# Performance work log

Measured on AMD Instinct MI355X. Metric: run time of the kernel, lower is better.

Reference implementation:

```python
import jax, jax.numpy as jnp
import numpy as np
from jax import lax

K = 2000      # node_num of GraphConvolution
H, W = 75, 100  # edge_region_feature spatial grid (from per-pixel concat loops)


def setup_inputs() -> dict:
    key = jax.random.key(0)
    k1, k2, k3, k4 = jax.random.split(key, 4)
    b, c = 8, 512
    edge_region_feature = jax.random.normal(k1, (b, c, H, W), dtype=jnp.float32)
    edge_region_predict = jax.random.normal(k2, (b, 3, H, W), dtype=jnp.float32)
    # GraphConvolution params: kaiming_normal_(fan_out) weights, zero bias
    w1 = jax.random.normal(k3, (512, 128), dtype=jnp.float32) * np.sqrt(2.0 / 128)
    b1 = jnp.zeros((K, 128), dtype=jnp.float32)
    w2 = jax.random.normal(k4, (128, 128), dtype=jnp.float32) * np.sqrt(2.0 / 128)
    b2 = jnp.zeros((K, 128), dtype=jnp.float32)
    return {"edge_region_feature": edge_region_feature,
            "edge_region_predict": edge_region_predict,
            "w1": w1, "b1": b1, "w2": w2, "b2": b2}


def reference(edge_region_feature, edge_region_predict, w1, b1, w2, b2):
    b, c = edge_region_feature.shape[0], edge_region_feature.shape[1]
    # block_feature built as: for x in range(W) for y in range(H) -> node n at (y=n%H, x=n//H)
    block = jnp.transpose(edge_region_feature, (0, 3, 2, 1)).reshape(b, W * H, c)  # (b, 7500, 512)

    # topk over channel-0 prediction, flattened row-major (idx = y*W + x)
    scores = edge_region_predict[:, 0, :, :].reshape(b, -1)            # (b, 7500)
    _vals, topk_idx = lax.top_k(scores, K)
    sorted_idx = jnp.sort(topk_idx, axis=1)                            # (b, 2000) int32

    # gather node features (replicates original's indexing of block_feature)
    node_map = jnp.take_along_axis(block, sorted_idx[:, :, None], axis=1)  # (b, 2000, 512)

    # generate_adjacent_map: decode positions with width=W, connect 8-neighborhood (+self)
    py = sorted_idx // W
    px = sorted_idx % W
    near_y = jnp.abs(py[:, :, None] - py[:, None, :]) <= 1
    near_x = jnp.abs(px[:, :, None] - px[:, None, :]) <= 1
    adj = (near_y & near_x).astype(jnp.float32)                        # (b, 2000, 2000)

    # node_feature_grouping = ReLU6 -> GCN(512->128) -> GCN(128->128)
    inp = jnp.clip(jnp.concatenate([adj, node_map], axis=2), 0.0, 6.0)  # ReLU6 on cat(adj, nodes)
    a = inp[:, :, :K]
    nf = inp[:, :, K:]
    # GCN1: A @ X @ W1 + b1  (in!=out -> no residual)
    x1 = jnp.einsum('bij,bjf->bif', a, nf) @ w1 + b1                   # (b, 2000, 128)
    # GCN2: A @ X1 @ W2 + b2 + X1 (in==out -> residual)
    x2 = jnp.einsum('bij,bjf->bif', a, x1) @ w2 + b2 + x1              # (b, 2000, 128)

    node_output_feature = jnp.tanh(x2)
    return node_output_feature, sorted_idx
```

## Files before the change

kernel.cpp:

```cpp
#include <hip/hip_runtime.h>
#include <cmath>

#define H_DIM 75
#define W_DIM 100
#define HW 7500
#define KSEL 2000
#define BATCH 8
#define CIN 512
#define FDIM 128

typedef short v4s __attribute__((ext_vector_type(4)));
typedef short v8s __attribute__((ext_vector_type(8)));
typedef float v16f __attribute__((ext_vector_type(16)));

__device__ __forceinline__ unsigned int map_key(float f) {
  unsigned int u = __float_as_uint(f);
  return (u & 0x80000000u) ? ~u : (u | 0x80000000u);
}

__device__ __forceinline__ float fast_tanh(float x) {
  float e = __expf(2.0f * x);
  return 1.0f - 2.0f * __builtin_amdgcn_rcpf(e + 1.0f);
}

__device__ __forceinline__ unsigned short bf16_rne(float v) {
  unsigned int u = __float_as_uint(v);
  unsigned int r = u + 0x7FFFu + ((u >> 16) & 1u);
  return (unsigned short)(r >> 16);
}
__device__ __forceinline__ float bf16_to_f(unsigned short h) {
  return __uint_as_float(((unsigned int)h) << 16);
}

__global__ __launch_bounds__(1024) void topk_nbr_kernel(
    const float* __restrict__ pred, const float* __restrict__ w1,
    const float* __restrict__ w2,
    int* __restrict__ off_ws, float* __restrict__ out_idx,
    unsigned short* __restrict__ nbr, unsigned char* __restrict__ cnt,
    unsigned short* __restrict__ w1t_hi, unsigned short* __restrict__ w1t_lo,
    unsigned short* __restrict__ w2t_hi, unsigned short* __restrict__ w2t_lo)
{
  __shared__ unsigned int keys[HW];
  __shared__ unsigned int whist[16 * 256];
  __shared__ unsigned int hist[256];
  __shared__ unsigned int partials[16];
  __shared__ unsigned int s_prefix, s_kth;
  const int tid = threadIdx.x;

  if (blockIdx.x >= BATCH) {
    int base = (blockIdx.x - BATCH) * 1024 + tid;
    for (int e = base; e < CIN * FDIM + FDIM * FDIM; e += 8 * 1024) {
      if (e < CIN * FDIM) {
        int k = e & (CIN - 1), f = e >> 9;
        float v = w1[k * FDIM + f];
        unsigned short hi = bf16_rne(v);
        unsigned short lo = bf16_rne(v - bf16_to_f(hi));
        w1t_hi[(size_t)f * CIN + k] = hi;
        w1t_lo[(size_t)f * CIN + k] = lo;
      } else {
        int e2 = e - CIN * FDIM;
        int k = e2 & (FDIM - 1), f = e2 >> 7;
        float v = w2[k * FDIM + f];
        unsigned short hi = bf16_rne(v);
        unsigned short lo = bf16_rne(v - bf16_to_f(hi));
        w2t_hi[(size_t)f * FDIM + k] = hi;
        w2t_lo[(size_t)f * FDIM + k] = lo;
      }
    }
    return;
  }

  const int b = blockIdx.x;
  const int lane = tid & 63, w = tid >> 6;
  const float* scores = pred + (size_t)b * 3 * HW;
  for (int i = tid; i < HW; i += 1024) keys[i] = map_key(scores[i]);
  if (tid == 0) { s_prefix = 0u; s_kth = KSEL; }
  __syncthreads();

  for (int shift = 24; shift >= 0; shift -= 8) {
    for (int i = tid; i < 16 * 256; i += 1024) whist[i] = 0u;
    __syncthreads();
    unsigned int pref = s_prefix;
    unsigned int maskhi = (shift == 24) ? 0u : (0xFFFFFFFFu << (shift + 8));
    for (int i = tid; i < HW; i += 1024) {
      unsigned int k = keys[i];
      if ((k & maskhi) == pref)
        atomicAdd(&whist[w * 256 + ((k >> shift) & 0xFFu)], 1u);
    }
    __syncthreads();
    if (tid < 256) {
      unsigned int s = 0;
      #pragma unroll
      for (int ww = 0; ww < 16; ++ww) s += whist[ww * 256 + tid];
      hist[tid] = s;
    }
    __syncthreads();
    if (tid < 64) {
      unsigned int b0 = hist[tid * 4], b1 = hist[tid * 4 + 1];
      unsigned int b2 = hist[tid * 4 + 2], b3 = hist[tid * 4 + 3];
      unsigned int kth = s_kth;
      unsigned int T = b0 + b1 + b2 + b3;
      #pragma unroll
      for (int off = 1; off < 64; off <<= 1) {
        unsigned int t = __shfl_down(T, off, 64);
        if (tid + off < 64) T += t;
      }
      unsigned int U = __shfl_down(T, 1, 64);
      if (tid == 63) U = 0u;
      unsigned int s3 = b3 + U, s2 = b2 + s3, s1 = b1 + s2, s0 = b0 + s1;
      if (s0 >= kth && s1 < kth) { s_prefix = pref | ((unsigned)(4 * tid + 0) << shift); s_kth = kth - s1; }
      if (s1 >= kth && s2 < kth) { s_prefix = pref | ((unsigned)(4 * tid + 1) << shift); s_kth = kth - s2; }
      if (s2 >= kth && s3 < kth) { s_prefix = pref | ((unsigned)(4 * tid + 2) << shift); s_kth = kth - s3; }
      if (s3 >= kth && U  < kth) { s_prefix = pref | ((unsigned)(4 * tid + 3) << shift); s_kth = kth - U; }
    }
    __syncthreads();
  }
  const unsigned int thresh = s_prefix;

  unsigned int local[8];
  unsigned int sum = 0;
  #pragma unroll
  for (int e = 0; e < 8; ++e) {
    int i = tid * 8 + e;
    unsigned int p = 0;
    if (i < HW) {
      unsigned int ky = keys[i];
      if (ky > thresh) p = 1u;
      else if (ky == thresh) p = (1u << 16);
    }
    local[e] = p; sum += p;
  }
  __syncthreads();
  short* pos_of  = (short*)keys;
  int*   s_idx_sh = (int*)((char*)keys + 15000);
  for (int i = tid; i < HW; i += 1024) pos_of[i] = -1;

  unsigned int inc = sum;
  #pragma unroll
  for (int off = 1; off < 64; off <<= 1) {
    unsigned int t = __shfl_up(inc, off, 64);
    if (lane >= off) inc += t;
  }
  if (lane == 63) partials[w] = inc;
  __syncthreads();
  if (tid < 16) {
    unsigned int v = partials[tid];
    #pragma unroll
    for (int off = 1; off < 16; off <<= 1) {
      unsigned int t = __shfl_up(v, off, 64);
      if (tid >= off) v += t;
    }
    partials[tid] = v;
  }
  __syncthreads();
  unsigned int total = partials[15];
  unsigned int run = (w ? partials[w - 1] : 0u) + inc - sum;
  unsigned int ties = (unsigned int)KSEL - (total & 0xFFFFu);
  #pragma unroll
  for (int e = 0; e < 8; ++e) {
    int i = tid * 8 + e;
    unsigned int p = local[e];
    unsigned int gt_pref = run & 0xFFFFu;
    unsigned int eq_pref = run >> 16;
    bool sel = (p & 1u) || (((p >> 16) != 0u) && eq_pref < ties);
    if (sel) {
      unsigned int pos = gt_pref + (eq_pref < ties ? eq_pref : ties);
      off_ws[b * KSEL + pos] = (i % H_DIM) * W_DIM + i / H_DIM;
      out_idx[b * KSEL + pos] = (float)i;
      s_idx_sh[pos] = i;
      pos_of[i] = (short)pos;
    }
    run += p;
  }
  __syncthreads();

  for (int i = tid; i < KSEL; i += 1024) {
    int q = s_idx_sh[i];
    int py = q / W_DIM, px = q % W_DIM;
    unsigned short tmp[9];
    int c = 0;
    #pragma unroll
    for (int dy = -1; dy <= 1; ++dy) {
      int y = py + dy;
      if ((unsigned)y >= (unsigned)H_DIM) continue;
      #pragma unroll
      for (int dx = -1; dx <= 1; ++dx) {
        int x = px + dx;
        if ((unsigned)x >= (unsigned)W_DIM) continue;
        short p = pos_of[y * W_DIM + x];
        if (p >= 0) tmp[c++] = (unsigned short)p;
      }
    }
    #pragma unroll
    for (int t = 0; t < 9; ++t)
      nbr[(size_t)(b * KSEL + i) * 9 + t] = (t < c) ? tmp[t] : (unsigned short)0;
    cnt[b * KSEL + i] = (unsigned char)c;
  }
}

__global__ __launch_bounds__(512) void gather_kernel(
    const float* __restrict__ feat, const int* __restrict__ off_ws,
    unsigned short* __restrict__ nft_hi, unsigned short* __restrict__ nft_lo)
{
  __shared__ __align__(16) float s_plane[HW];
  const int b = blockIdx.y;
  const int c = blockIdx.x;
  const int tid = threadIdx.x;
  const float4* p4 = (const float4*)(feat + ((size_t)b * CIN + c) * HW);
  float4* sp4 = (float4*)s_plane;
  #pragma unroll
  for (int i = tid; i < HW / 4; i += 512)
    sp4[i] = p4[i];
  __syncthreads();
  if (tid < KSEL / 4) {
    const uint4* o4 = (const uint4*)off_ws + (size_t)b * (KSEL / 4);
    uint4 o = o4[tid];
    float v0 = fminf(fmaxf(s_plane[o.x], 0.f), 6.f);
    float v1 = fminf(fmaxf(s_plane[o.y], 0.f), 6.f);
    float v2 = fminf(fmaxf(s_plane[o.z], 0.f), 6.f);
    float v3 = fminf(fmaxf(s_plane[o.w], 0.f), 6.f);
    ushort4 h, l;
    h.x = bf16_rne(v0); l.x = bf16_rne(v0 - bf16_to_f(h.x));
    h.y = bf16_rne(v1); l.y = bf16_rne(v1 - bf16_to_f(h.y));
    h.z = bf16_rne(v2); l.z = bf16_rne(v2 - bf16_to_f(h.z));
    h.w = bf16_rne(v3); l.w = bf16_rne(v3 - bf16_to_f(h.w));
    size_t row = ((size_t)b * CIN + c) * KSEL;
    ((ushort4*)&nft_hi[row])[tid] = h;
    ((ushort4*)&nft_lo[row])[tid] = l;
  }
}

__global__ __launch_bounds__(256) void gemm1_mfma(
    const unsigned short* __restrict__ nft_hi,
    const unsigned short* __restrict__ nft_lo,
    const unsigned short* __restrict__ w1t_hi,
    const unsigned short* __restrict__ w1t_lo,
    float* __restrict__ G)
{
  __shared__ unsigned short a_hi[2][64][20], a_lo[2][64][20];
  const int b = blockIdx.y;
  const int n0 = blockIdx.x * 64;
  const int tid = threadIdx.x;
  const int lane = tid & 63, w = tid >> 6;
  const int wr = w & 1, wc = w >> 1;
  const int q = lane >> 5, m = lane & 31;
  v16f acc0, acc1;
  #pragma unroll
  for (int i = 0; i < 16; ++i) { acc0[i] = 0.f; acc1[i] = 0.f; }
  const unsigned short* nh = nft_hi + (size_t)b * CIN * KSEL;
  const unsigned short* nl = nft_lo + (size_t)b * CIN * KSEL;
  const int an = wr * 32 + m;
  const int f0 = wc * 64 + m;
  const int n_st = tid & 63, ks = (tid >> 6) * 4;

  #pragma unroll
  for (int j = 0; j < 4; ++j) {
    size_t gi = (size_t)(ks + j) * KSEL + n0 + n_st;
    a_hi[0][n_st][ks + j] = nh[gi];
    a_lo[0][n_st][ks + j] = nl[gi];
  }
  __syncthreads();

  for (int k0 = 0; k0 < CIN; k0 += 16) {
    const int p = (k0 >> 4) & 1;
    if (k0 + 16 < CIN) {
      #pragma unroll
      for (int j = 0; j < 4; ++j) {
        size_t gi = (size_t)(k0 + 16 + ks + j) * KSEL + n0 + n_st;
        a_hi[p ^ 1][n_st][ks + j] = nh[gi];
        a_lo[p ^ 1][n_st][ks + j] = nl[gi];
      }
    }
    v4s ah0 = *(const v4s*)&a_hi[p][an][q * 8];
    v4s ah1 = *(const v4s*)&a_hi[p][an][q * 8 + 4];
    v4s al0 = *(const v4s*)&a_lo[p][an][q * 8];
    v4s al1 = *(const v4s*)&a_lo[p][an][q * 8 + 4];
    v8s avh = __builtin_shufflevector(ah0, ah1, 0, 1, 2, 3, 4, 5, 6, 7);
    v8s avl = __builtin_shufflevector(al0, al1, 0, 1, 2, 3, 4, 5, 6, 7);
    v8s b0h = *(const v8s*)&w1t_hi[(size_t)f0 * CIN + k0 + q * 8];
    v8s b0l = *(const v8s*)&w1t_lo[(size_t)f0 * CIN + k0 + q * 8];
    v8s b1h = *(const v8s*)&w1t_hi[(size_t)(f0 + 32) * CIN + k0 + q * 8];
    v8s b1l = *(const v8s*)&w1t_lo[(size_t)(f0 + 32) * CIN + k0 + q * 8];
    acc0 = __builtin_amdgcn_mfma_f32_32x32x16_bf16(avh, b0h, acc0, 0, 0, 0);
    acc0 = __builtin_amdgcn_mfma_f32_32x32x16_bf16(avh, b0l, acc0, 0, 0, 0);
    acc0 = __builtin_amdgcn_mfma_f32_32x32x16_bf16(avl, b0h, acc0, 0, 0, 0);
    acc1 = __builtin_amdgcn_mfma_f32_32x32x16_bf16(avh, b1h, acc1, 0, 0, 0);
    acc1 = __builtin_amdgcn_mfma_f32_32x32x16_bf16(avh, b1l, acc1, 0, 0, 0);
    acc1 = __builtin_amdgcn_mfma_f32_32x32x16_bf16(avl, b1h, acc1, 0, 0, 0);
    __syncthreads();
  }
  float* ob = G + (size_t)b * KSEL * FDIM;
  #pragma unroll
  for (int reg = 0; reg < 16; ++reg) {
    int row = n0 + wr * 32 + (reg & 3) + 8 * (reg >> 2) + 4 * q;
    if (row < KSEL) {
      ob[(size_t)row * FDIM + f0]      = acc0[reg];
      ob[(size_t)row * FDIM + f0 + 32] = acc1[reg];
    }
  }
}

__global__ __launch_bounds__(256) void x1_kernel(
    const float* __restrict__ G, const float* __restrict__ b1,
    const unsigned short* __restrict__ nbr, const unsigned char* __restrict__ cnt,
    float* __restrict__ x1, unsigned short* __restrict__ x1h,
    unsigned short* __restrict__ x1l)
{
  const int g = threadIdx.x >> 5, lane = threadIdx.x & 31;
  const int node = blockIdx.x * 8 + g;
  const int bb = blockIdx.y;
  const size_t bi = (size_t)bb * KSEL + node;
  const unsigned short* nb = nbr + bi * 9;
  unsigned short idx[9];
  #pragma unroll
  for (int t = 0; t < 9; ++t) idx[t] = nb[t];
  const int c = cnt[bi];
  const float4* G4 = (const float4*)G + (size_t)bb * KSEL * 32;
  float4 v[9];
  #pragma unroll
  for (int t = 0; t < 9; ++t) v[t] = G4[(size_t)idx[t] * 32 + lane];
  float4 acc = ((const float4*)b1)[node * 32 + lane];
  #pragma unroll
  for (int t = 0; t < 9; ++t) {
    float mk = (t < c) ? 1.f : 0.f;
    acc.x = fmaf(v[t].x, mk, acc.x);
    acc.y = fmaf(v[t].y, mk, acc.y);
    acc.z = fmaf(v[t].z, mk, acc.z);
    acc.w = fmaf(v[t].w, mk, acc.w);
  }
  ((float4*)x1)[bi * 32 + lane] = acc;
  ushort4 h, l;
  h.x = bf16_rne(acc.x); l.x = bf16_rne(acc.x - bf16_to_f(h.x));
  h.y = bf16_rne(acc.y); l.y = bf16_rne(acc.y - bf16_to_f(h.y));
  h.z = bf16_rne(acc.z); l.z = bf16_rne(acc.z - bf16_to_f(h.z));
  h.w = bf16_rne(acc.w); l.w = bf16_rne(acc.w - bf16_to_f(h.w));
  ((ushort4*)x1h)[bi * 32 + lane] = h;
  ((ushort4*)x1l)[bi * 32 + lane] = l;
}

__global__ __launch_bounds__(256) void gemm2_mfma(
    const unsigned short* __restrict__ x1h,
    const unsigned short* __restrict__ x1l,
    const unsigned short* __restrict__ w2t_hi,
    const unsigned short* __restrict__ w2t_lo,
    float* __restrict__ Hm)
{
  const int b = blockIdx.y;
  const int n0 = blockIdx.x * 64;
  const int tid = threadIdx.x;
  const int lane = tid & 63, w = tid >> 6;
  const int wr = w & 1, wc = w >> 1;
  const int q = lane >> 5, m = lane & 31;
  int arow = n0 + wr * 32 + m;
  if (arow > KSEL - 1) arow = KSEL - 1;
  const unsigned short* xh = x1h + ((size_t)b * KSEL + arow) * FDIM;
  const unsigned short* xl = x1l + ((size_t)b * KSEL + arow) * FDIM;
  const int f0 = wc * 64 + m;
  v16f acc0, acc1;
  #pragma unroll
  for (int i = 0; i < 16; ++i) { acc0[i] = 0.f; acc1[i] = 0.f; }
  #pragma unroll
  for (int k0 = 0; k0 < FDIM; k0 += 16) {
    v8s avh = *(const v8s*)&xh[k0 + q * 8];
    v8s avl = *(const v8s*)&xl[k0 + q * 8];
    v8s b0h = *(const v8s*)&w2t_hi[(size_t)f0 * FDIM + k0 + q * 8];
    v8s b0l = *(const v8s*)&w2t_lo[(size_t)f0 * FDIM + k0 + q * 8];
    v8s b1h = *(const v8s*)&w2t_hi[(size_t)(f0 + 32) * FDIM + k0 + q * 8];
    v8s b1l = *(const v8s*)&w2t_lo[(size_t)(f0 + 32) * FDIM + k0 + q * 8];
    acc0 = __builtin_amdgcn_mfma_f32_32x32x16_bf16(avh, b0h, acc0, 0, 0, 0);
    acc0 = __builtin_amdgcn_mfma_f32_32x32x16_bf16(avh, b0l, acc0, 0, 0, 0);
    acc0 = __builtin_amdgcn_mfma_f32_32x32x16_bf16(avl, b0h, acc0, 0, 0, 0);
    acc1 = __builtin_amdgcn_mfma_f32_32x32x16_bf16(avh, b1h, acc1, 0, 0, 0);
    acc1 = __builtin_amdgcn_mfma_f32_32x32x16_bf16(avh, b1l, acc1, 0, 0, 0);
    acc1 = __builtin_amdgcn_mfma_f32_32x32x16_bf16(avl, b1h, acc1, 0, 0, 0);
  }
  float* ob = Hm + (size_t)b * KSEL * FDIM;
  #pragma unroll
  for (int reg = 0; reg < 16; ++reg) {
    int row = n0 + wr * 32 + (reg & 3) + 8 * (reg >> 2) + 4 * q;
    if (row < KSEL) {
      ob[(size_t)row * FDIM + f0]      = acc0[reg];
      ob[(size_t)row * FDIM + f0 + 32] = acc1[reg];
    }
  }
}

__global__ __launch_bounds__(256) void out_kernel(
    const float* __restrict__ Hm, const float* __restrict__ x1,
    const float* __restrict__ b2,
    const unsigned short* __restrict__ nbr, const unsigned char* __restrict__ cnt,
    float* __restrict__ out)
{
  const int g = threadIdx.x >> 5, lane = threadIdx.x & 31;
  const int node = blockIdx.x * 8 + g;
  const int bb = blockIdx.y;
  const size_t bi = (size_t)bb * KSEL + node;
  const unsigned short* nb = nbr + bi * 9;
  unsigned short idx[9];
  #pragma unroll
  for (int t = 0; t < 9; ++t) idx[t] = nb[t];
  const int c = cnt[bi];
  const float4* H4 = (const float4*)Hm + (size_t)bb * KSEL * 32;
  float4 v[9];
  #pragma unroll
  for (int t = 0; t < 9; ++t) v[t] = H4[(size_t)idx[t] * 32 + lane];
  float4 acc = ((const float4*)b2)[node * 32 + lane];
  float4 xv = ((const float4*)x1)[bi * 32 + lane];
  acc.x += xv.x; acc.y += xv.y; acc.z += xv.z; acc.w += xv.w;
  #pragma unroll
  for (int t = 0; t < 9; ++t) {
    float mk = (t < c) ? 1.f : 0.f;
    acc.x = fmaf(v[t].x, mk, acc.x);
    acc.y = fmaf(v[t].y, mk, acc.y);
    acc.z = fmaf(v[t].z, mk, acc.z);
    acc.w = fmaf(v[t].w, mk, acc.w);
  }
  float4 r;
  r.x = fast_tanh(acc.x); r.y = fast_tanh(acc.y);
  r.z = fast_tanh(acc.z); r.w = fast_tanh(acc.w);
  ((float4*)out)[bi * 32 + lane] = r;
}

extern "C" void kernel_launch(void* const* d_in, const int* in_sizes, int n_in,
                              void* d_out, int out_size, void* d_ws, size_t ws_size,
                              hipStream_t stream) {
  const float* feat = (const float*)d_in[0];
  const float* pred = (const float*)d_in[1];
  const float* w1   = (const float*)d_in[2];
  const float* b1   = (const float*)d_in[3];
  const float* w2   = (const float*)d_in[4];
  const float* b2   = (const float*)d_in[5];
  float* out0 = (float*)d_out;
  float* out_idx = out0 + (size_t)BATCH * KSEL * FDIM;

  char* ws = (char*)d_ws;
  int*            off_ws = (int*)(ws + 0);
  unsigned short* nbr    = (unsigned short*)(ws + 64256);
  unsigned char*  cnt    = (unsigned char*)(ws + 352512);
  float*          G      = (float*)(ws + 368640);
  char*           R      = ws + 8560640;
  unsigned short* nft_hi = (unsigned short*)R;
  unsigned short* nft_lo = (unsigned short*)(R + 16384000);
  unsigned short* w1t_hi = (unsigned short*)(R + 32768256);
  unsigned short* w1t_lo = (unsigned short*)(R + 32899328);
  unsigned short* w2t_hi = (unsigned short*)(R + 33030656);
  unsigned short* w2t_lo = (unsigned short*)(R + 33063424);
  float*          x1     = (float*)R;
  float*          Hm     = (float*)(R + 8388608);
  unsigned short* x1h    = (unsigned short*)(R + 16777216);
  unsigned short* x1l    = (unsigned short*)(R + 20873472);

  topk_nbr_kernel<<<BATCH + 8, 1024, 0, stream>>>(
      pred, w1, w2, off_ws, out_idx, nbr, cnt, w1t_hi, w1t_lo, w2t_hi, w2t_lo);
  gather_kernel<<<dim3(CIN, BATCH), 512, 0, stream>>>(feat, off_ws, nft_hi, nft_lo);
  gemm1_mfma<<<dim3(32, BATCH), 256, 0, stream>>>(nft_hi, nft_lo, w1t_hi, w1t_lo, G);
  x1_kernel<<<dim3(KSEL / 8, BATCH), 256, 0, stream>>>(G, b1, nbr, cnt, x1, x1h, x1l);
  gemm2_mfma<<<dim3(32, BATCH), 256, 0, stream>>>(x1h, x1l, w2t_hi, w2t_lo, Hm);
  out_kernel<<<dim3(KSEL / 8, BATCH), 256, 0, stream>>>(Hm, x1, b2, nbr, cnt, out0);
}
```

Measured before the change: 263.7 us.

## Fuse feature gather into GEMM1 and sparse aggregation into GEMM2

Removes the separate gather kernel: GEMM1 now reads the selected node features directly from the input tensor via the offset table, applies ReLU6 and splits them into bf16 hi/lo in-register before staging to shared memory. It also folds the x1 neighbor-aggregation kernel into GEMM2, which builds the bf16 x1 tile in XOR-swizzled shared memory instead of round-tripping through global buffers. This cuts two launches and the large nft_hi/nft_lo intermediate writes and reads. The cost is that GEMM1's A loads become strided scalar reads (stride HW floats per channel) from the original feature layout, with only 256 blocks doing that gathering work.

```diff
diff --git a/kernel.cpp b/kernel.cpp
--- a/kernel.cpp
+++ b/kernel.cpp
@@ -198,41 +198,8 @@
   }
 }
 
-__global__ __launch_bounds__(512) void gather_kernel(
+__global__ __launch_bounds__(256) void gemm1_fused(
     const float* __restrict__ feat, const int* __restrict__ off_ws,
-    unsigned short* __restrict__ nft_hi, unsigned short* __restrict__ nft_lo)
-{
-  __shared__ __align__(16) float s_plane[HW];
-  const int b = blockIdx.y;
-  const int c = blockIdx.x;
-  const int tid = threadIdx.x;
-  const float4* p4 = (const float4*)(feat + ((size_t)b * CIN + c) * HW);
-  float4* sp4 = (float4*)s_plane;
-  #pragma unroll
-  for (int i = tid; i < HW / 4; i += 512)
-    sp4[i] = p4[i];
-  __syncthreads();
-  if (tid < KSEL / 4) {
-    const uint4* o4 = (const uint4*)off_ws + (size_t)b * (KSEL / 4);
-    uint4 o = o4[tid];
-    float v0 = fminf(fmaxf(s_plane[o.x], 0.f), 6.f);
-    float v1 = fminf(fmaxf(s_plane[o.y], 0.f), 6.f);
-    float v2 = fminf(fmaxf(s_plane[o.z], 0.f), 6.f);
-    float v3 = fminf(fmaxf(s_plane[o.w], 0.f), 6.f);
-    ushort4 h, l;
-    h.x = bf16_rne(v0); l.x = bf16_rne(v0 - bf16_to_f(h.x));
-    h.y = bf16_rne(v1); l.y = bf16_rne(v1 - bf16_to_f(h.y));
-    h.z = bf16_rne(v2); l.z = bf16_rne(v2 - bf16_to_f(h.z));
-    h.w = bf16_rne(v3); l.w = bf16_rne(v3 - bf16_to_f(h.w));
-    size_t row = ((size_t)b * CIN + c) * KSEL;
-    ((ushort4*)&nft_hi[row])[tid] = h;
-    ((ushort4*)&nft_lo[row])[tid] = l;
-  }
-}
-
-__global__ __launch_bounds__(256) void gemm1_mfma(
-    const unsigned short* __restrict__ nft_hi,
-    const unsigned short* __restrict__ nft_lo,
     const unsigned short* __restrict__ w1t_hi,
     const unsigned short* __restrict__ w1t_lo,
     float* __restrict__ G)
@@ -247,17 +214,20 @@
   v16f acc0, acc1;
   #pragma unroll
   for (int i = 0; i < 16; ++i) { acc0[i] = 0.f; acc1[i] = 0.f; }
-  const unsigned short* nh = nft_hi + (size_t)b * CIN * KSEL;
-  const unsigned short* nl = nft_lo + (size_t)b * CIN * KSEL;
   const int an = wr * 32 + m;
   const int f0 = wc * 64 + m;
   const int n_st = tid & 63, ks = (tid >> 6) * 4;
+  int nidx = n0 + n_st;
+  if (nidx > KSEL - 1) nidx = KSEL - 1;
+  const float* fb = feat + (size_t)b * CIN * HW + off_ws[b * KSEL + nidx];
 
   #pragma unroll
   for (int j = 0; j < 4; ++j) {
-    size_t gi = (size_t)(ks + j) * KSEL + n0 + n_st;
-    a_hi[0][n_st][ks + j] = nh[gi];
-    a_lo[0][n_st][ks + j] = nl[gi];
+    float v = fb[(size_t)(ks + j) * HW];
+    v = fminf(fmaxf(v, 0.f), 6.f);
+    unsigned short hi = bf16_rne(v);
+    a_hi[0][n_st][ks + j] = hi;
+    a_lo[0][n_st][ks + j] = bf16_rne(v - bf16_to_f(hi));
   }
   __syncthreads();
 
@@ -266,9 +236,11 @@
     if (k0 + 16 < CIN) {
       #pragma unroll
       for (int j = 0; j < 4; ++j) {
-        size_t gi = (size_t)(k0 + 16 + ks + j) * KSEL + n0 + n_st;
-        a_hi[p ^ 1][n_st][ks + j] = nh[gi];
-        a_lo[p ^ 1][n_st][ks + j] = nl[gi];
+        float v = fb[(size_t)(k0 + 16 + ks + j) * HW];
+        v = fminf(fmaxf(v, 0.f), 6.f);
+        unsigned short hi = bf16_rne(v);
+        a_hi[p ^ 1][n_st][ks + j] = hi;
+        a_lo[p ^ 1][n_st][ks + j] = bf16_rne(v - bf16_to_f(hi));
       }
     }
     v4s ah0 = *(const v4s*)&a_hi[p][an][q * 8];
@@ -300,69 +272,69 @@
   }
 }
 
-__global__ __launch_bounds__(256) void x1_kernel(
+__global__ __launch_bounds__(256) void gemm2_fused(
     const float* __restrict__ G, const float* __restrict__ b1,
     const unsigned short* __restrict__ nbr, const unsigned char* __restrict__ cnt,
-    float* __restrict__ x1, unsigned short* __restrict__ x1h,
-    unsigned short* __restrict__ x1l)
-{
-  const int g = threadIdx.x >> 5, lane = threadIdx.x & 31;
-  const int node = blockIdx.x * 8 + g;
-  const int bb = blockIdx.y;
-  const size_t bi = (size_t)bb * KSEL + node;
-  const unsigned short* nb = nbr + bi * 9;
-  unsigned short idx[9];
-  #pragma unroll
-  for (int t = 0; t < 9; ++t) idx[t] = nb[t];
-  const int c = cnt[bi];
-  const float4* G4 = (const float4*)G + (size_t)bb * KSEL * 32;
-  float4 v[9];
-  #pragma unroll
-  for (int t = 0; t < 9; ++t) v[t] = G4[(size_t)idx[t] * 32 + lane];
-  float4 acc = ((const float4*)b1)[node * 32 + lane];
-  #pragma unroll
-  for (int t = 0; t < 9; ++t) {
-    float mk = (t < c) ? 1.f : 0.f;
-    acc.x = fmaf(v[t].x, mk, acc.x);
-    acc.y = fmaf(v[t].y, mk, acc.y);
-    acc.z = fmaf(v[t].z, mk, acc.z);
-    acc.w = fmaf(v[t].w, mk, acc.w);
-  }
-  ((float4*)x1)[bi * 32 + lane] = acc;
-  ushort4 h, l;
-  h.x = bf16_rne(acc.x); l.x = bf16_rne(acc.x - bf16_to_f(h.x));
-  h.y = bf16_rne(acc.y); l.y = bf16_rne(acc.y - bf16_to_f(h.y));
-  h.z = bf16_rne(acc.z); l.z = bf16_rne(acc.z - bf16_to_f(h.z));
-  h.w = bf16_rne(acc.w); l.w = bf16_rne(acc.w - bf16_to_f(h.w));
-  ((ushort4*)x1h)[bi * 32 + lane] = h;
-  ((ushort4*)x1l)[bi * 32 + lane] = l;
-}
-
-__global__ __launch_bounds__(256) void gemm2_mfma(
-    const unsigned short* __restrict__ x1h,
-    const unsigned short* __restrict__ x1l,
     const unsigned short* __restrict__ w2t_hi,
     const unsigned short* __restrict__ w2t_lo,
-    float* __restrict__ Hm)
+    float* __restrict__ x1, float* __restrict__ Hm)
 {
+  __shared__ __align__(16) unsigned short xh[64][FDIM];
+  __shared__ __align__(16) unsigned short xl[64][FDIM];
   const int b = blockIdx.y;
   const int n0 = blockIdx.x * 64;
   const int tid = threadIdx.x;
+  const int g = tid >> 5, lane32 = tid & 31;
+  const float4* G4 = (const float4*)G + (size_t)b * KSEL * 32;
+
+  #pragma unroll 2
+  for (int rr = 0; rr < 8; ++rr) {
+    const int r = rr * 8 + g;
+    const int node = n0 + r;
+    const int nodec = (node > KSEL - 1) ? KSEL - 1 : node;
+    const size_t bi = (size_t)b * KSEL + nodec;
+    const unsigned short* nb = nbr + bi * 9;
+    unsigned short idx[9];
+    #pragma unroll
+    for (int t = 0; t < 9; ++t) idx[t] = nb[t];
+    const int c = cnt[bi];
+    float4 v[9];
+    #pragma unroll
+    for (int t = 0; t < 9; ++t) v[t] = G4[(size_t)idx[t] * 32 + lane32];
+    float4 acc = ((const float4*)b1)[nodec * 32 + lane32];
+    #pragma unroll
+    for (int t = 0; t < 9; ++t) {
+      float mk = (t < c) ? 1.f : 0.f;
+      acc.x = fmaf(v[t].x, mk, acc.x);
+      acc.y = fmaf(v[t].y, mk, acc.y);
+      acc.z = fmaf(v[t].z, mk, acc.z);
+      acc.w = fmaf(v[t].w, mk, acc.w);
+    }
+    if (node < KSEL) ((float4*)x1)[bi * 32 + lane32] = acc;
+    ushort4 h, l;
+    h.x = bf16_rne(acc.x); l.x = bf16_rne(acc.x - bf16_to_f(h.x));
+    h.y = bf16_rne(acc.y); l.y = bf16_rne(acc.y - bf16_to_f(h.y));
+    h.z = bf16_rne(acc.z); l.z = bf16_rne(acc.z - bf16_to_f(h.z));
+    h.w = bf16_rne(acc.w); l.w = bf16_rne(acc.w - bf16_to_f(h.w));
+    const int cs = (lane32 * 4) ^ ((r & 15) << 3);
+    *(ushort4*)&xh[r][cs] = h;
+    *(ushort4*)&xl[r][cs] = l;
+  }
+  __syncthreads();
+
   const int lane = tid & 63, w = tid >> 6;
   const int wr = w & 1, wc = w >> 1;
   const int q = lane >> 5, m = lane & 31;
-  int arow = n0 + wr * 32 + m;
-  if (arow > KSEL - 1) arow = KSEL - 1;
-  const unsigned short* xh = x1h + ((size_t)b * KSEL + arow) * FDIM;
-  const unsigned short* xl = x1l + ((size_t)b * KSEL + arow) * FDIM;
+  const int ar = wr * 32 + m;
   const int f0 = wc * 64 + m;
   v16f acc0, acc1;
   #pragma unroll
   for (int i = 0; i < 16; ++i) { acc0[i] = 0.f; acc1[i] = 0.f; }
   #pragma unroll
   for (int k0 = 0; k0 < FDIM; k0 += 16) {
-    v8s avh = *(const v8s*)&xh[k0 + q * 8];
-    v8s avl = *(const v8s*)&xl[k0 + q * 8];
+    const int ac = (k0 + q * 8) ^ ((ar & 15) << 3);
+    v8s avh = *(const v8s*)&xh[ar][ac];
+    v8s avl = *(const v8s*)&xl[ar][ac];
     v8s b0h = *(const v8s*)&w2t_hi[(size_t)f0 * FDIM + k0 + q * 8];
     v8s b0l = *(const v8s*)&w2t_lo[(size_t)f0 * FDIM + k0 + q * 8];
     v8s b1h = *(const v8s*)&w2t_hi[(size_t)(f0 + 32) * FDIM + k0 + q * 8];
@@ -438,23 +410,16 @@
   unsigned short* nbr    = (unsigned short*)(ws + 64256);
   unsigned char*  cnt    = (unsigned char*)(ws + 352512);
   float*          G      = (float*)(ws + 368640);
-  char*           R      = ws + 8560640;
-  unsigned short* nft_hi = (unsigned short*)R;
-  unsigned short* nft_lo = (unsigned short*)(R + 16384000);
-  unsigned short* w1t_hi = (unsigned short*)(R + 32768256);
-  unsigned short* w1t_lo = (unsigned short*)(R + 32899328);
-  unsigned short* w2t_hi = (unsigned short*)(R + 33030656);
-  unsigned short* w2t_lo = (unsigned short*)(R + 33063424);
-  float*          x1     = (float*)R;
-  float*          Hm     = (float*)(R + 8388608);
-  unsigned short* x1h    = (unsigned short*)(R + 16777216);
-  unsigned short* x1l    = (unsigned short*)(R + 20873472);
+  float*          x1     = (float*)(ws + 8560640);
+  float*          Hm     = (float*)(ws + 16752640);
+  unsigned short* w1t_hi = (unsigned short*)(ws + 24944896);
+  unsigned short* w1t_lo = (unsigned short*)(ws + 25075968);
+  unsigned short* w2t_hi = (unsigned short*)(ws + 25207040);
+  unsigned short* w2t_lo = (unsigned short*)(ws + 25239808);
 
   topk_nbr_kernel<<<BATCH + 8, 1024, 0, stream>>>(
       pred, w1, w2, off_ws, out_idx, nbr, cnt, w1t_hi, w1t_lo, w2t_hi, w2t_lo);
-  gather_kernel<<<dim3(CIN, BATCH), 512, 0, stream>>>(feat, off_ws, nft_hi, nft_lo);
-  gemm1_mfma<<<dim3(32, BATCH), 256, 0, stream>>>(nft_hi, nft_lo, w1t_hi, w1t_lo, G);
-  x1_kernel<<<dim3(KSEL / 8, BATCH), 256, 0, stream>>>(G, b1, nbr, cnt, x1, x1h, x1l);
-  gemm2_mfma<<<dim3(32, BATCH), 256, 0, stream>>>(x1h, x1l, w2t_hi, w2t_lo, Hm);
+  gemm1_fused<<<dim3(32, BATCH), 256, 0, stream>>>(feat, off_ws, w1t_hi, w1t_lo, G);
+  gemm2_fused<<<dim3(32, BATCH), 256, 0, stream>>>(G, b1, nbr, cnt, w2t_hi, w2t_lo, x1, Hm);
   out_kernel<<<dim3(KSEL / 8, BATCH), 256, 0, stream>>>(Hm, x1, b2, nbr, cnt, out0);
 }
```

Measured after the change: 282.2 us. 1.07x slower.
